# Performance work log

Hardware: AMD Instinct MI355X
Metric: run time of the kernel (lower is better)

## Reference

```python
import jax, jax.numpy as jnp
import numpy as np

B, S, D_IN, D_OUT = 4, 2048, 4096, 4096
ALPHA, INSCALE = 0.001, 0.05


def setup_inputs() -> dict:
    key = jax.random.key(0)
    kx, kw = jax.random.split(key)
    x = jax.random.normal(kx, (B, S, D_IN), dtype=jnp.float32)
    # int8 weight in [-127, 126], matching torch.randint(-127, 127, ...)
    weight = jax.random.randint(kw, (D_OUT, D_IN), -127, 127, dtype=jnp.int32).astype(jnp.int8)
    return {
        "x": x,
        "weight": weight,
        "alpha": jnp.float32(ALPHA),
        "inscale": jnp.float32(INSCALE),
    }


def reference(x, weight, alpha, inscale):
    x_shape = x.shape
    xf = x.reshape(-1, x_shape[-1])                        # [M, K]
    # dynamic per-tensor int8 quantization of activations
    q = jnp.clip(jnp.round(xf / inscale), -128, 127).astype(jnp.int8)
    y = jax.lax.dot_general(
        q, weight,
        dimension_numbers=(((1,), (1,)), ((), ())),
        preferred_element_type=jnp.int32,
    )
    # dequant epilogue: scalar alpha scale -> fp32
    y = y.astype(jnp.float32) * alpha
    return y.reshape(*x_shape[:-1], -1)                    # [B, S, N]
```

## Files before the change

kernel.cpp:

```cpp
#include <hip/hip_runtime.h>
#include <cstdint>


typedef int v4i  __attribute__((ext_vector_type(4)));
typedef int v16i __attribute__((ext_vector_type(16)));

#define BM 256
#define BN 256
#define BKB 64
#define LDS_TILE (BM * BKB)
#define LDS_BUF  (2 * LDS_TILE)
#define NBUF 3

__global__ void prep_kernel(const float* __restrict__ x,
                            signed char* __restrict__ q,
                            const int* __restrict__ w32,
                            signed char* __restrict__ w8,
                            const float* __restrict__ inscale_ptr,
                            int nq, int total) {
    const float s = *inscale_ptr;
    const int stride = gridDim.x * blockDim.x;
    for (int i = blockIdx.x * blockDim.x + threadIdx.x; i < total; i += stride) {
        if (i < nq) {
            float4 f = ((const float4*)x)[i];
            union { signed char c[4]; int v; } u;
            float vals[4] = {f.x, f.y, f.z, f.w};
#pragma unroll
            for (int e = 0; e < 4; ++e) {
                float r = rintf(vals[e] / s);
                r = fminf(fmaxf(r, -128.0f), 127.0f);
                u.c[e] = (signed char)(int)r;
            }
            ((int*)q)[i] = u.v;
        } else {
            const int j = i - nq;
            int4 w = ((const int4*)w32)[j];
            union { signed char c[4]; int v; } u;
            u.c[0] = (signed char)w.x;
            u.c[1] = (signed char)w.y;
            u.c[2] = (signed char)w.z;
            u.c[3] = (signed char)w.w;
            ((int*)w8)[j] = u.v;
        }
    }
}

__device__ __forceinline__ void async16(void* lds, const void* g) {
    __builtin_amdgcn_global_load_lds(
        (const __attribute__((address_space(1))) void*)g,
        (__attribute__((address_space(3))) void*)lds,
        16, 0, 0);
}

__global__ __launch_bounds__(512, 2)
void w8a8_gemm(const signed char* __restrict__ A,
               const signed char* __restrict__ Bw,
               float* __restrict__ C,
               const float* __restrict__ alpha_ptr,
               int M, int N, int K) {
    __shared__ signed char lds[NBUF * LDS_BUF];

    const int t    = threadIdx.x;
    const int lane = t & 63;
    const int wave = t >> 6;
    const int wm   = (wave >> 2) * 128;
    const int wn   = (wave & 3) * 64;

    const int nbx   = N / BN;
    const int swz   = ((int)blockIdx.x & 7) * ((int)gridDim.x >> 3)
                    + ((int)blockIdx.x >> 3);
    const int tileM = (swz / nbx) * BM;
    const int tileN = (swz % nbx) * BN;

    const int srow = t >> 2;
    const int sg   = (t & 3) ^ ((t >> 3) & 3);
    const size_t aOff0 = (size_t)(tileM + srow)       * K + sg * 16;
    const size_t aOff1 = (size_t)(tileM + 128 + srow) * K + sg * 16;
    const size_t bOff0 = (size_t)(tileN + srow)       * K + sg * 16;
    const size_t bOff1 = (size_t)(tileN + 128 + srow) * K + sg * 16;
    const int ldst = t * 16;

    auto stageA = [&](int kt, int buf) {
        const size_t ko = (size_t)kt * BKB;
        signed char* d = &lds[buf * LDS_BUF];
        async16(d + ldst,        A + aOff0 + ko);
        async16(d + 8192 + ldst, A + aOff1 + ko);
    };
    auto stageB = [&](int kt, int buf) {
        const size_t ko = (size_t)kt * BKB;
        signed char* d = &lds[buf * LDS_BUF + LDS_TILE];
        async16(d + ldst,        Bw + bOff0 + ko);
        async16(d + 8192 + ldst, Bw + bOff1 + ko);
    };

    const int mrow  = lane & 31;
    const int khalf = lane >> 5;
    const int fswz  = (mrow >> 1) & 3;
    const int offS0 = ((0 + khalf) ^ fswz) * 16;
    const int offS1 = ((2 + khalf) ^ fswz) * 16;
    int arow[4], brow[2];
#pragma unroll
    for (int im = 0; im < 4; ++im) arow[im] = (wm + im * 32 + mrow) * BKB;
#pragma unroll
    for (int jn = 0; jn < 2; ++jn) brow[jn] = LDS_TILE + (wn + jn * 32 + mrow) * BKB;

    v16i acc[4][2] = {};

    auto phase = [&](const signed char* cb, int offp) {
        v4i a[4], b[2];
#pragma unroll
        for (int im = 0; im < 4; ++im)
            a[im] = *(const v4i*)(cb + arow[im] + offp);
#pragma unroll
        for (int jn = 0; jn < 2; ++jn)
            b[jn] = *(const v4i*)(cb + brow[jn] + offp);
        asm volatile("s_barrier" ::: "memory");
        __builtin_amdgcn_s_setprio(1);
#pragma unroll
        for (int im = 0; im < 4; ++im)
#pragma unroll
            for (int jn = 0; jn < 2; ++jn)
                acc[im][jn] = __builtin_amdgcn_mfma_i32_32x32x32_i8(
                    a[im], b[jn], acc[im][jn], 0, 0, 0);
        __builtin_amdgcn_s_setprio(0);
    };

    stageA(0, 0); stageB(0, 0);
    stageA(1, 1); stageB(1, 1);
    asm volatile("s_waitcnt vmcnt(4)" ::: "memory");
    asm volatile("s_barrier" ::: "memory");

    const int NT = K / BKB;
    int bc = 0, sb = 2;
#pragma unroll 1
    for (int kt = 0; kt < NT; ++kt) {
        const bool doStage = (kt + 2) < NT;
        const signed char* cb = &lds[bc * LDS_BUF];

        if (doStage) stageA(kt + 2, sb);
        phase(cb, offS0);
        asm volatile("s_barrier" ::: "memory");

        if (doStage) stageB(kt + 2, sb);
        phase(cb, offS1);

        if (doStage) asm volatile("s_waitcnt vmcnt(4)" ::: "memory");
        else         asm volatile("s_waitcnt vmcnt(0)" ::: "memory");
        asm volatile("s_barrier" ::: "memory");

        bc = (bc == NBUF - 1) ? 0 : bc + 1;
        sb = (sb == NBUF - 1) ? 0 : sb + 1;
    }

    const float alpha = *alpha_ptr;
    const int ccol  = lane & 31;
    const int rquad = khalf * 4;
#pragma unroll
    for (int im = 0; im < 4; ++im) {
#pragma unroll
        for (int jn = 0; jn < 2; ++jn) {
            const int baseRow = tileM + wm + im * 32;
            const int col     = tileN + wn + jn * 32 + ccol;
#pragma unroll
            for (int reg = 0; reg < 16; ++reg) {
                const int row = baseRow + (reg & 3) + 8 * (reg >> 2) + rquad;
                C[(size_t)row * N + col] = (float)acc[im][jn][reg] * alpha;
            }
        }
    }
}

extern "C" void kernel_launch(void* const* d_in, const int* in_sizes, int n_in,
                              void* d_out, int out_size, void* d_ws, size_t ws_size,
                              hipStream_t stream) {
    const float* x       = (const float*)d_in[0];
    const int*   w32     = (const int*)d_in[1];
    const float* alpha   = (const float*)d_in[2];
    const float* inscale = (const float*)d_in[3];
    float*       out     = (float*)d_out;

    const int K = 4096;
    const int N = 4096;
    const int M = in_sizes[0] / K;

    signed char* q  = (signed char*)d_ws;
    signed char* w8 = (signed char*)d_ws + (size_t)M * K;

    const int nq    = (M * K) / 4;
    const int total = nq + (N * K) / 4;
    prep_kernel<<<2048, 256, 0, stream>>>(x, q, w32, w8, inscale, nq, total);

    dim3 grid((M / BM) * (N / BN));
    w8a8_gemm<<<grid, 512, 0, stream>>>(q, w8, out, alpha, M, N, K);
}
```

Baseline: 413.7 us.

## Merge two k-phases into one per iteration with fewer barriers

Each iteration now loads both k-halves of LDS fragments up front and issues both async global-to-LDS stages together. It then runs all 16 MFMAs in one block. This removes the three inline-asm s_barriers inside the loop, leaving only the end-of-iteration barrier, and replaces the asm barriers with the builtin. The aim is less synchronisation overhead and longer uninterrupted MFMA runs. The cost is more registers for the fragments and less interleaving between global staging and compute.

```diff
diff --git a/kernel.cpp b/kernel.cpp
--- a/kernel.cpp
+++ b/kernel.cpp
@@ -96,8 +96,8 @@
     const int mrow  = lane & 31;
     const int khalf = lane >> 5;
     const int fswz  = (mrow >> 1) & 3;
-    const int offS0 = ((0 + khalf) ^ fswz) * 16;
-    const int offS1 = ((2 + khalf) ^ fswz) * 16;
+    const int offS[2] = { ((0 + khalf) ^ fswz) * 16,
+                          ((2 + khalf) ^ fswz) * 16 };
     int arow[4], brow[2];
 #pragma unroll
     for (int im = 0; im < 4; ++im) arow[im] = (wm + im * 32 + mrow) * BKB;
@@ -106,29 +106,10 @@
 
     v16i acc[4][2] = {};
 
-    auto phase = [&](const signed char* cb, int offp) {
-        v4i a[4], b[2];
-#pragma unroll
-        for (int im = 0; im < 4; ++im)
-            a[im] = *(const v4i*)(cb + arow[im] + offp);
-#pragma unroll
-        for (int jn = 0; jn < 2; ++jn)
-            b[jn] = *(const v4i*)(cb + brow[jn] + offp);
-        asm volatile("s_barrier" ::: "memory");
-        __builtin_amdgcn_s_setprio(1);
-#pragma unroll
-        for (int im = 0; im < 4; ++im)
-#pragma unroll
-            for (int jn = 0; jn < 2; ++jn)
-                acc[im][jn] = __builtin_amdgcn_mfma_i32_32x32x32_i8(
-                    a[im], b[jn], acc[im][jn], 0, 0, 0);
-        __builtin_amdgcn_s_setprio(0);
-    };
-
     stageA(0, 0); stageB(0, 0);
     stageA(1, 1); stageB(1, 1);
     asm volatile("s_waitcnt vmcnt(4)" ::: "memory");
-    asm volatile("s_barrier" ::: "memory");
+    __builtin_amdgcn_s_barrier();
 
     const int NT = K / BKB;
     int bc = 0, sb = 2;
@@ -137,16 +118,34 @@
         const bool doStage = (kt + 2) < NT;
         const signed char* cb = &lds[bc * LDS_BUF];
 
-        if (doStage) stageA(kt + 2, sb);
-        phase(cb, offS0);
-        asm volatile("s_barrier" ::: "memory");
+        v4i a[2][4], b[2][2];
+#pragma unroll
+        for (int s = 0; s < 2; ++s) {
+            const int offp = offS[s];
+#pragma unroll
+            for (int im = 0; im < 4; ++im)
+                a[s][im] = *(const v4i*)(cb + arow[im] + offp);
+#pragma unroll
+            for (int jn = 0; jn < 2; ++jn)
+                b[s][jn] = *(const v4i*)(cb + brow[jn] + offp);
+        }
 
-        if (doStage) stageB(kt + 2, sb);
-        phase(cb, offS1);
+        if (doStage) { stageA(kt + 2, sb); stageB(kt + 2, sb); }
+
+        __builtin_amdgcn_s_setprio(1);
+#pragma unroll
+        for (int s = 0; s < 2; ++s)
+#pragma unroll
+            for (int im = 0; im < 4; ++im)
+#pragma unroll
+                for (int jn = 0; jn < 2; ++jn)
+                    acc[im][jn] = __builtin_amdgcn_mfma_i32_32x32x32_i8(
+                        a[s][im], b[s][jn], acc[im][jn], 0, 0, 0);
+        __builtin_amdgcn_s_setprio(0);
 
         if (doStage) asm volatile("s_waitcnt vmcnt(4)" ::: "memory");
         else         asm volatile("s_waitcnt vmcnt(0)" ::: "memory");
-        asm volatile("s_barrier" ::: "memory");
+        __builtin_amdgcn_s_barrier();
 
         bc = (bc == NBUF - 1) ? 0 : bc + 1;
         sb = (sb == NBUF - 1) ? 0 : sb + 1;
```

Measured after the change: 406.3 us. About the same (-1.8%).
